# Kernel tuning notes

Measured on AMD Instinct MI355X. Metric: run time of the kernel, lower is better.

The kernel has to match this reference:

```python
import jax, jax.numpy as jnp
import numpy as np

INF = 1e30  # sentinel for 'unreached' cost
MAX_ITERS = 512


def setup_inputs() -> dict:
    key = jax.random.key(0)
    img = jax.random.uniform(key, (3, 2048, 2048), dtype=jnp.float32)
    return {"img": img}


def _sobel_mag(gray):
    # gray: [H,W] -> gradient magnitude [H,W] (the 'processing_filter')
    kx = jnp.array([[-1.0, 0.0, 1.0], [-2.0, 0.0, 2.0], [-1.0, 0.0, 1.0]], gray.dtype)
    k = jnp.stack([kx, kx.T])[:, None]  # [2,1,3,3]
    g = jax.lax.conv_general_dilated(gray[None, None], k, (1, 1), 'SAME')[0]  # [2,H,W]
    return jnp.sqrt(g[0] ** 2 + g[1] ** 2)


def _neighbor_min(c):
    # min over 4-connected neighbors, INF padding at borders
    big_r = jnp.full((1, c.shape[1]), INF, c.dtype)
    big_c = jnp.full((c.shape[0], 1), INF, c.dtype)
    n = jnp.concatenate([big_r, c[:-1]], 0)
    s = jnp.concatenate([c[1:], big_r], 0)
    w = jnp.concatenate([big_c, c[:, :-1]], 1)
    e = jnp.concatenate([c[:, 1:], big_c], 1)
    return jnp.minimum(jnp.minimum(n, s), jnp.minimum(w, e))


def _relax(cost, img):
    # minimax-path (flood-level) relaxation: cost[p] = min(cost[p], max(min_nbr_cost, img[p]))
    return jnp.minimum(cost, jnp.maximum(_neighbor_min(cost), img))


def _watershed2(img, markers):
    # marker-based watershed on topography `img` with labels {1,2}.
    # Label of p = argmin over seed sets of the minimax path cost (flooding level),
    # which matches skimage.segmentation.watershed region assignment (4-connectivity).
    c1 = jnp.where(markers == 1, img, jnp.float32(INF))
    c2 = jnp.where(markers == 2, img, jnp.float32(INF))

    def cond(st):
        _, _, i, ch = st
        return jnp.logical_and(ch, i < MAX_ITERS)

    def body(st):
        c1, c2, i, _ = st
        n1 = _relax(c1, img)
        n2 = _relax(c2, img)
        ch = jnp.logical_or(jnp.any(n1 < c1), jnp.any(n2 < c2))
        return n1, n2, i + 1, ch

    c1, c2, _, _ = jax.lax.while_loop(cond, body, (c1, c2, jnp.int32(0), jnp.bool_(True)))
    return jnp.where(c2 < c1, jnp.float32(2.0), jnp.float32(1.0))


def _forward(img):
    gray = jnp.einsum('chw,c->hw', img, jnp.array([0.2989, 0.587, 0.114], img.dtype))
    filter_res = _sobel_mag(gray)  # [H,W]
    q_hi = jnp.quantile(filter_res, 0.9925)
    q_lo = jnp.quantile(filter_res, 0.9825)
    # torch sets 2 first, then 1, so pixels satisfying both end up as 1
    markers = jnp.where(filter_res <= q_lo, 1, jnp.where(filter_res >= q_hi, 2, 0))
    labels = _watershed2(gray, markers)[None]  # [1,H,W], values in {1,2}
    labels = labels - labels.min()
    return labels / labels.max()


def reference(img):
    return _forward(img)
```

## Files before the change

kernel.cpp:

```cpp
#include <hip/hip_runtime.h>
#include <hip/hip_cooperative_groups.h>

#define HH 2048
#define WW 2048
#define NPX (HH*WW)
#define INFV 1e30f
#define TS 128
#define NT 16
#define NTL 256
#define CY 32

namespace cg = cooperative_groups;

__device__ __forceinline__ void BARL(){
  __builtin_amdgcn_sched_barrier(0);
  asm volatile("s_waitcnt lgkmcnt(0)" ::: "memory");
  __builtin_amdgcn_s_barrier();
  __builtin_amdgcn_sched_barrier(0);
}

__device__ __forceinline__ float sobel_at(const float* __restrict__ g, int y, int x){
  float a00,a01,a02,a10,a12,a20,a21,a22;
  if (y>0 && y<HH-1 && x>0 && x<WW-1){
    const float* p = g + (size_t)(y-1)*WW + x;
    a00=p[-1]; a01=p[0]; a02=p[1];
    p += WW;   a10=p[-1];          a12=p[1];
    p += WW;   a20=p[-1]; a21=p[0]; a22=p[1];
  } else {
    auto at=[&](int yy,int xx)->float{
      return (yy<0||yy>=HH||xx<0||xx>=WW)?0.0f:g[(size_t)yy*WW+xx];
    };
    a00=at(y-1,x-1); a01=at(y-1,x); a02=at(y-1,x+1);
    a10=at(y,  x-1);                a12=at(y,  x+1);
    a20=at(y+1,x-1); a21=at(y+1,x); a22=at(y+1,x+1);
  }
  float gx = __fadd_rn(__fadd_rn(__fsub_rn(a02,a00), __fmul_rn(2.0f,__fsub_rn(a12,a10))), __fsub_rn(a22,a20));
  float gy = __fadd_rn(__fadd_rn(__fsub_rn(a20,a00), __fmul_rn(2.0f,__fsub_rn(a21,a01))), __fsub_rn(a22,a02));
  return sqrtf(__fadd_rn(__fmul_rn(gx,gx),__fmul_rn(gy,gy)));
}

__global__ void gray_kernel(const float* __restrict__ img, float* __restrict__ gray){
  const float* R=img; const float* G=img+NPX; const float* B=img+2*(size_t)NPX;
  for (int i=blockIdx.x*blockDim.x+threadIdx.x; i<NPX; i+=gridDim.x*blockDim.x){
    gray[i] = __fadd_rn(__fadd_rn(__fmul_rn(0.2989f,R[i]),__fmul_rn(0.587f,G[i])),__fmul_rn(0.114f,B[i]));
  }
}

__global__ void sobel_hist1(const float* __restrict__ gray, float* __restrict__ fr,
                            unsigned* __restrict__ hist){
  __shared__ unsigned h[4*2048];
  for (int i=threadIdx.x;i<4*2048;i+=blockDim.x) h[i]=0;
  __syncthreads();
  const int rep=(threadIdx.x&3)*2048;
  for (int i=blockIdx.x*blockDim.x+threadIdx.x; i<NPX; i+=gridDim.x*blockDim.x){
    int y=i>>11, x=i&(WW-1);
    float f=sobel_at(gray,y,x);
    fr[i]=f;
    unsigned key=__float_as_uint(f);
    atomicAdd(&h[rep+(key>>21)],1u);
  }
  __syncthreads();
  for (int i=threadIdx.x;i<2048;i+=blockDim.x){
    unsigned s=h[i]+h[i+2048]+h[i+4096]+h[i+6144];
    if (s) atomicAdd(&hist[i],s);
  }
}

__global__ void hist_l2(const float* __restrict__ fr, const unsigned* __restrict__ sel1,
                        unsigned* __restrict__ hist2){
  __shared__ unsigned h[4*2048];
  __shared__ unsigned sb[4];
  if (threadIdx.x<4) sb[threadIdx.x]=sel1[threadIdx.x];
  for (int i=threadIdx.x;i<4*2048;i+=blockDim.x) h[i]=0;
  __syncthreads();
  for (int i=blockIdx.x*blockDim.x+threadIdx.x; i<NPX; i+=gridDim.x*blockDim.x){
    unsigned key=__float_as_uint(fr[i]);
    unsigned b=key>>21, sub=(key>>10)&0x7FFu;
    #pragma unroll
    for (int k=0;k<4;++k) if (b==sb[k]) atomicAdd(&h[k*2048+sub],1u);
  }
  __syncthreads();
  for (int i=threadIdx.x;i<4*2048;i+=blockDim.x){ unsigned s=h[i]; if (s) atomicAdd(&hist2[i],s); }
}

__global__ void hist_l3(const float* __restrict__ fr, const unsigned* __restrict__ sel1,
                        const unsigned* __restrict__ sel2, unsigned* __restrict__ hist3){
  __shared__ unsigned h[4*1024];
  __shared__ unsigned pf[4];
  if (threadIdx.x<4) pf[threadIdx.x]=(sel1[threadIdx.x]<<11)|sel2[threadIdx.x];
  for (int i=threadIdx.x;i<4*1024;i+=blockDim.x) h[i]=0;
  __syncthreads();
  for (int i=blockIdx.x*blockDim.x+threadIdx.x; i<NPX; i+=gridDim.x*blockDim.x){
    unsigned key=__float_as_uint(fr[i]);
    unsigned p22=key>>10, sub=key&0x3FFu;
    #pragma unroll
    for (int k=0;k<4;++k) if (p22==pf[k]) atomicAdd(&h[k*1024+sub],1u);
  }
  __syncthreads();
  for (int i=threadIdx.x;i<4*1024;i+=blockDim.x){ unsigned s=h[i]; if (s) atomicAdd(&hist3[i],s); }
}

__global__ void scan_l1(const unsigned* __restrict__ hist, unsigned* __restrict__ sel1,
                        unsigned* __restrict__ rem1){
  __shared__ unsigned part[1024];
  const int t=threadIdx.x;
  unsigned a=hist[2*t], b=hist[2*t+1];
  part[t]=a+b; __syncthreads();
  for (int off=1;off<1024;off<<=1){
    unsigned add=(t>=off)?part[t-off]:0u; __syncthreads();
    part[t]+=add; __syncthreads();
  }
  unsigned before=(t>0)?part[t-1]:0u;
  const unsigned R[4]={4120902u,4120903u,4162845u,4162846u};
  unsigned cum=before;
  #pragma unroll
  for (int i=0;i<4;++i) if (R[i]>=cum && R[i]<cum+a){ sel1[i]=2*t;   rem1[i]=R[i]-cum; }
  cum+=a;
  #pragma unroll
  for (int i=0;i<4;++i) if (R[i]>=cum && R[i]<cum+b){ sel1[i]=2*t+1; rem1[i]=R[i]-cum; }
}

__global__ void scan_l2(const unsigned* __restrict__ hist2, const unsigned* __restrict__ rem1,
                        unsigned* __restrict__ sel2, unsigned* __restrict__ rem2){
  __shared__ unsigned part[1024];
  const int t=threadIdx.x;
  for (int i=0;i<4;++i){
    const unsigned* hh=hist2+i*2048;
    unsigned a=hh[2*t], b=hh[2*t+1];
    part[t]=a+b; __syncthreads();
    for (int off=1;off<1024;off<<=1){
      unsigned add=(t>=off)?part[t-off]:0u; __syncthreads();
      part[t]+=add; __syncthreads();
    }
    unsigned before=(t>0)?part[t-1]:0u;
    unsigned r=rem1[i], cum=before;
    if (r>=cum && r<cum+a){ sel2[i]=2*t;   rem2[i]=r-cum; }
    cum+=a;
    if (r>=cum && r<cum+b){ sel2[i]=2*t+1; rem2[i]=r-cum; }
    __syncthreads();
  }
}

__global__ void scan_l3(const unsigned* __restrict__ hist3, const unsigned* __restrict__ sel1,
                        const unsigned* __restrict__ sel2, const unsigned* __restrict__ rem2,
                        float* __restrict__ scal){
  __shared__ unsigned part[1024];
  __shared__ float vals[4];
  const int t=threadIdx.x;
  for (int i=0;i<4;++i){
    unsigned c=hist3[i*1024+t];
    part[t]=c; __syncthreads();
    for (int off=1;off<1024;off<<=1){
      unsigned add=(t>=off)?part[t-off]:0u; __syncthreads();
      part[t]+=add; __syncthreads();
    }
    unsigned before=(t>0)?part[t-1]:0u;
    unsigned r=rem2[i];
    if (r>=before && r<before+c){
      unsigned key=(sel1[i]<<21)|(sel2[i]<<10)|(unsigned)t;
      vals[i]=__uint_as_float(key);
    }
    __syncthreads();
  }
  if (t==0){
    scal[0]=__fadd_rn(__fmul_rn(vals[0],0.25f),__fmul_rn(vals[1],0.75f));
    scal[1]=__fadd_rn(__fmul_rn(vals[2],0.25f),__fmul_rn(vals[3],0.75f));
  }
}

__global__ void init_cost(const float* __restrict__ gray, const float* frbuf,
                          const float* __restrict__ scal,
                          float* c1out, float* __restrict__ c2out){
  const float qlo=scal[0], qhi=scal[1];
  for (int i=blockIdx.x*blockDim.x+threadIdx.x; i<NPX; i+=gridDim.x*blockDim.x){
    float f=frbuf[i];
    float g=gray[i];
    bool m1 = (f<=qlo);
    bool m2 = (!m1) && (f>=qhi);
    c1out[i] = m1 ? g : INFV;
    c2out[i] = (m1|m2) ? g : INFV;
  }
}


#define HSCAN_LR(va,vb,gA,gB,hl) do{ \
  float ql_=gA[j], qh_=va[j]; \
  qh_=fminf(vb[j],fmaxf(gB[j],qh_)); ql_=fmaxf(gB[j],ql_); \
  _Pragma("unroll") \
  for (int d_=1;d_<64;d_<<=1){ \
    float pl_=__shfl_up(ql_,(unsigned)d_), ph_=__shfl_up(qh_,(unsigned)d_); \
    if (c>=d_){ qh_=fminf(qh_,fmaxf(ql_,ph_)); ql_=fmaxf(ql_,pl_); } \
  } \
  float E_=fminf(qh_,fmaxf(ql_,(hl))); \
  float In_=__shfl_up(E_,1u); if(c==0) In_=(hl); \
  float na_=fminf(va[j],fmaxf(gA[j],In_)); if(na_<va[j]){va[j]=na_;ch=true;} \
  float nb_=fminf(vb[j],fmaxf(gB[j],na_)); if(nb_<vb[j]){vb[j]=nb_;ch=true;} \
}while(0)

#define HSCAN_RL(va,vb,gA,gB,hr) do{ \
  float ql_=gB[j], qh_=vb[j]; \
  qh_=fminf(va[j],fmaxf(gA[j],qh_)); ql_=fmaxf(gA[j],ql_); \
  _Pragma("unroll") \
  for (int d_=1;d_<64;d_<<=1){ \
    float pl_=__shfl_down(ql_,(unsigned)d_), ph_=__shfl_down(qh_,(unsigned)d_); \
    if (c+d_<64){ qh_=fminf(qh_,fmaxf(ql_,ph_)); ql_=fmaxf(ql_,pl_); } \
  } \
  float E_=fminf(qh_,fmaxf(ql_,(hr))); \
  float In_=__shfl_down(E_,1u); if(c==63) In_=(hr); \
  float nb_=fminf(vb[j],fmaxf(gB[j],In_)); if(nb_<vb[j]){vb[j]=nb_;ch=true;} \
  float na_=fminf(va[j],fmaxf(gA[j],nb_)); if(na_<va[j]){va[j]=na_;ch=true;} \
}while(0)

#define VCOMP_DN(va,gA,Larr,Harr,XX) { float ql_=gA[0], qh_=va[0]; \
  _Pragma("unroll") for (int jj_=1;jj_<8;++jj_){ qh_=fminf(va[jj_],fmaxf(gA[jj_],qh_)); ql_=fmaxf(gA[jj_],ql_);} \
  Larr[w][XX]=ql_; Harr[w][XX]=qh_; }

#define VCOMP_UP(va,gA,Larr,Harr,XX) { float ql_=gA[7], qh_=va[7]; \
  _Pragma("unroll") for (int jj_=6;jj_>=0;--jj_){ qh_=fminf(va[jj_],fmaxf(gA[jj_],qh_)); ql_=fmaxf(gA[jj_],ql_);} \
  Larr[w][XX]=ql_; Harr[w][XX]=qh_; }

#define VAPPLY_DN(va,gA,Larr,XX) { float In_=Larr[w][XX]; \
  _Pragma("unroll") for (int jj_=0;jj_<8;++jj_){ float nv_=fminf(va[jj_],fmaxf(In_,gA[jj_])); if(nv_<va[jj_]){va[jj_]=nv_;ch=true;} In_=nv_; } }

#define VAPPLY_UP(va,gA,Larr,XX) { float In_=Larr[w][XX]; \
  _Pragma("unroll") for (int jj_=7;jj_>=0;--jj_){ float nv_=fminf(va[jj_],fmaxf(In_,gA[jj_])); if(nv_<va[jj_]){va[jj_]=nv_;ch=true;} In_=nv_; } }

#define CHAIN_DN(Harr,Larr,HT) { float E=HALO[HT][x]; \
  _Pragma("unroll") for (int b_=0;b_<16;++b_){ float I=E; E=fminf(Harr[b_][x],fmaxf(Larr[b_][x],I)); Larr[b_][x]=I; } }

#define CHAIN_UP(Harr,Larr,HB) { float E=HALO[HB][x]; \
  _Pragma("unroll") for (int b_=15;b_>=0;--b_){ float I=E; E=fminf(Harr[b_][x],fmaxf(Larr[b_][x],I)); Larr[b_][x]=I; } }

#define HFIELD(va,vb,IHL,IHR) do{ \
  _Pragma("unroll") \
  for (int j=0;j<8;++j){ \
    const int r_=(w<<3)|j; \
    const float hl=HALO[IHL][r_], hr=HALO[IHR][r_]; \
    { float la_=__shfl_up(vb[j],1u); if(c==0) la_=hl; \
      bool p_=__any((fminf(va[j],fmaxf(la_,ga[j]))<va[j])||(fminf(vb[j],fmaxf(va[j],gb[j]))<vb[j])); \
      if (p_){ HSCAN_LR(va,vb,ga,gb,hl); } } \
    { float ra_=__shfl_down(va[j],1u); if(c==63) ra_=hr; \
      bool p_=__any((fminf(vb[j],fmaxf(ra_,gb[j]))<vb[j])||(fminf(va[j],fmaxf(vb[j],ga[j]))<va[j])); \
      if (p_){ HSCAN_RL(va,vb,ga,gb,hr); } } \
  } \
}while(0)

#define ASTORE(p,v) __hip_atomic_store((p),(v),__ATOMIC_RELAXED,__HIP_MEMORY_SCOPE_AGENT)
#define ALOAD(p)    __hip_atomic_load((p),__ATOMIC_RELAXED,__HIP_MEMORY_SCOPE_AGENT)

__global__ void __launch_bounds__(1024,4)
tile_solve(float* __restrict__ c1g, float* __restrict__ cg, const float* __restrict__ grayg)
{
  __shared__ float DNL1[16][128], DNH1[16][128], DNL2[16][128], DNH2[16][128];
  __shared__ float UPL1[16][128], UPH1[16][128], UPL2[16][128], UPH2[16][128];
  __shared__ float HALO[8][128];
  __shared__ int VN1[2],HN1[2],VN2[2],HN2[2];
  const int tid=threadIdx.x, w=tid>>6, c=tid&63;
  const int oty=blockIdx.x>>5, otx=blockIdx.x&31;
  const int wy0=oty*64-32, wx0=otx*64-32, x0=c<<1;
  HALO[tid>>7][tid&127]=INFV;
  if (tid==0){ VN1[0]=1;HN1[0]=1;VN2[0]=1;HN2[0]=1;
               VN1[1]=0;HN1[1]=0;VN2[1]=0;HN2[1]=0; }
  float v1a[8],v1b[8],v2a[8],v2b[8],ga[8],gb[8];
  const int gx=wx0+x0;
  const bool cok=(gx>=0)&&(gx+1<WW);
  #pragma unroll
  for (int j=0;j<8;++j){
    const int gy=wy0+(w<<3)+j;
    const bool rok=(gy>=0)&&(gy<HH);
    if (rok&&cok){
      const size_t b=(size_t)gy*WW+gx;
      float2 t1=*(const float2*)(c1g+b);
      float2 t2=*(const float2*)(cg+b);
      float2 tg=*(const float2*)(grayg+b);
      v1a[j]=t1.x; v1b[j]=t1.y; v2a[j]=t2.x; v2b[j]=t2.y; ga[j]=tg.x; gb[j]=tg.y;
    } else if (rok){
      const bool aok=(gx>=0)&&(gx<WW), bok=(gx+1>=0)&&(gx+1<WW);
      const size_t b=(size_t)gy*WW;
      v1a[j]=aok?c1g[b+gx]:INFV;   v1b[j]=bok?c1g[b+gx+1]:INFV;
      v2a[j]=aok?cg [b+gx]:INFV;   v2b[j]=bok?cg [b+gx+1]:INFV;
      ga [j]=aok?grayg[b+gx]:INFV; gb [j]=bok?grayg[b+gx+1]:INFV;
    } else {
      v1a[j]=INFV;v1b[j]=INFV;v2a[j]=INFV;v2b[j]=INFV;ga[j]=INFV;gb[j]=INFV;
    }
  }
  __syncthreads();
  for (int cyc=0; cyc<64; ++cyc){
    const int cur=cyc&1, nxt=cur^1;
    const int vn1=VN1[cur], hn1=HN1[cur], vn2=VN2[cur], hn2=HN2[cur];
    if (!(vn1|hn1|vn2|hn2)) break;
    if (vn1){
      VCOMP_DN(v1a,ga,DNL1,DNH1,x0) VCOMP_DN(v1b,gb,DNL1,DNH1,x0+1)
      VCOMP_UP(v1a,ga,UPL1,UPH1,x0) VCOMP_UP(v1b,gb,UPL1,UPH1,x0+1)
    }
    if (vn2){
      VCOMP_DN(v2a,ga,DNL2,DNH2,x0) VCOMP_DN(v2b,gb,DNL2,DNH2,x0+1)
      VCOMP_UP(v2a,ga,UPL2,UPH2,x0) VCOMP_UP(v2b,gb,UPL2,UPH2,x0+1)
    }
    __syncthreads();
    if (w<8){
      const int x=((w&1)<<6)|c;
      const bool go=(w>>2)?(vn2!=0):(vn1!=0);
      if (go){
        switch(w>>1){
          case 0: CHAIN_DN(DNH1,DNL1,0) break;
          case 1: CHAIN_UP(UPH1,UPL1,2) break;
          case 2: CHAIN_DN(DNH2,DNL2,1) break;
          default:CHAIN_UP(UPH2,UPL2,3) break;
        }
      }
    }
    __syncthreads();
    if (vn1){ bool ch=false;
      VAPPLY_DN(v1a,ga,DNL1,x0) VAPPLY_DN(v1b,gb,DNL1,x0+1)
      VAPPLY_UP(v1a,ga,UPL1,x0) VAPPLY_UP(v1b,gb,UPL1,x0+1)
      if (ch) HN1[nxt]=1;
    }
    if (hn1){ bool ch=false;
      HFIELD(v1a,v1b,4,6);
      if (ch) VN1[nxt]=1;
    }
    if (vn2){ bool ch=false;
      VAPPLY_DN(v2a,ga,DNL2,x0) VAPPLY_DN(v2b,gb,DNL2,x0+1)
      VAPPLY_UP(v2a,ga,UPL2,x0) VAPPLY_UP(v2b,gb,UPL2,x0+1)
      if (ch) HN2[nxt]=1;
    }
    if (hn2){ bool ch=false;
      HFIELD(v2a,v2b,5,7);
      if (ch) VN2[nxt]=1;
    }
    if (tid==0){ VN1[cur]=0; HN1[cur]=0; VN2[cur]=0; HN2[cur]=0; }
    __syncthreads();
  }
  if (w>=4 && w<12 && c>=16 && c<48){
    #pragma unroll
    for (int j=0;j<8;++j){
      const int gy=wy0+(w<<3)+j;
      const size_t b=(size_t)gy*WW+gx;
      float2 o1; o1.x=v1a[j]; o1.y=v1b[j];
      float2 o2; o2.x=v2a[j]; o2.y=v2b[j];
      *(float2*)(c1g+b)=o1;
      *(float2*)(cg +b)=o2;
    }
  }
}

#define CYCLE(HV,CUR,NXT) do{ \
  if (hsrc){ \
    if (HV < HALO[harr][hx]){ \
      HALO[harr][hx]=HV; \
      if (harr<4){ if (harr&1) VN2[NXT]=1; else VN1[NXT]=1; } \
      else       { if (harr&1) HN2[NXT]=1; else HN1[NXT]=1; } \
    } \
    HV=ALOAD(hsrc); \
  } \
  const int vn1=VN1[CUR], hn1=HN1[CUR], vn2=VN2[CUR], hn2=HN2[CUR]; \
  if (!(vn1|hn1|vn2|hn2)){ \
    BARL(); \
  } else { \
    if (vn1){ \
      VCOMP_DN(v1a,ga,DNL1,DNH1,x0) VCOMP_DN(v1b,gb,DNL1,DNH1,x0+1) \
      VCOMP_UP(v1a,ga,UPL1,UPH1,x0) VCOMP_UP(v1b,gb,UPL1,UPH1,x0+1) \
    } \
    if (vn2){ \
      VCOMP_DN(v2a,ga,DNL2,DNH2,x0) VCOMP_DN(v2b,gb,DNL2,DNH2,x0+1) \
      VCOMP_UP(v2a,ga,UPL2,UPH2,x0) VCOMP_UP(v2b,gb,UPL2,UPH2,x0+1) \
    } \
    BARL(); \
    if (w<8){ \
      const int x=((w&1)<<6)|c; \
      const bool go = (w>>2) ? (vn2!=0) : (vn1!=0); \
      if (go){ \
        switch(w>>1){ \
          case 0: CHAIN_DN(DNH1,DNL1,0) break; \
          case 1: CHAIN_UP(UPH1,UPL1,2) break; \
          case 2: CHAIN_DN(DNH2,DNL2,1) break; \
          default:CHAIN_UP(UPH2,UPL2,3) break; \
        } \
      } \
    } \
    BARL(); \
    bool chf1=false, chf2=false; \
    if (vn1){ bool ch=false; \
      VAPPLY_DN(v1a,ga,DNL1,x0) VAPPLY_DN(v1b,gb,DNL1,x0+1) \
      VAPPLY_UP(v1a,ga,UPL1,x0) VAPPLY_UP(v1b,gb,UPL1,x0+1) \
      if (ch){ chf1=true; HN1[NXT]=1; } \
    } \
    if (hn1){ bool ch=false; \
      HFIELD(v1a,v1b,4,6); \
      if (ch){ chf1=true; VN1[NXT]=1; } \
    } \
    if (vn2){ bool ch=false; \
      VAPPLY_DN(v2a,ga,DNL2,x0) VAPPLY_DN(v2b,gb,DNL2,x0+1) \
      VAPPLY_UP(v2a,ga,UPL2,x0) VAPPLY_UP(v2b,gb,UPL2,x0+1) \
      if (ch){ chf2=true; HN2[NXT]=1; } \
    } \
    if (hn2){ bool ch=false; \
      HFIELD(v2a,v2b,5,7); \
      if (ch){ chf2=true; VN2[NXT]=1; } \
    } \
    if (chf1|chf2){ \
      if (w==0){ const int eb=(tile*4+0)*128; \
        if(chf1){ ASTORE(EB1+eb+x0,v1a[0]); ASTORE(EB1+eb+x0+1,v1b[0]); } \
        if(chf2){ ASTORE(EB2+eb+x0,v2a[0]); ASTORE(EB2+eb+x0+1,v2b[0]); } } \
      if (w==15){ const int eb=(tile*4+1)*128; \
        if(chf1){ ASTORE(EB1+eb+x0,v1a[7]); ASTORE(EB1+eb+x0+1,v1b[7]); } \
        if(chf2){ ASTORE(EB2+eb+x0,v2a[7]); ASTORE(EB2+eb+x0+1,v2b[7]); } } \
      if (c==0){ const int eb=(tile*4+2)*128+(w<<3); \
        _Pragma("unroll") \
        for (int j=0;j<8;++j){ if(chf1)ASTORE(EB1+eb+j,v1a[j]); if(chf2)ASTORE(EB2+eb+j,v2a[j]); } } \
      if (c==63){ const int eb=(tile*4+3)*128+(w<<3); \
        _Pragma("unroll") \
        for (int j=0;j<8;++j){ if(chf1)ASTORE(EB1+eb+j,v1b[j]); if(chf2)ASTORE(EB2+eb+j,v2b[j]); } } \
      wflag=1; \
    } \
    if (tid==0){ VN1[CUR]=0; HN1[CUR]=0; VN2[CUR]=0; HN2[CUR]=0; } \
    BARL(); \
  } \
}while(0)

__global__ void __launch_bounds__(1024,4)
ws_solve(float* __restrict__ c1g, const float* __restrict__ grayg, float* outg,
         int* __restrict__ flagIt)
{
  __shared__ float DNL1[16][128], DNH1[16][128], DNL2[16][128], DNH2[16][128];
  __shared__ float UPL1[16][128], UPH1[16][128], UPL2[16][128], UPH2[16][128];
  __shared__ float HALO[8][128];
  __shared__ int VN1[2],HN1[2],VN2[2],HN2[2];
  __shared__ int wflag;
  cg::grid_group grid = cg::this_grid();
  const int tid=threadIdx.x, w=tid>>6, c=tid&63;
  const int xcd=blockIdx.x&7, idx=blockIdx.x>>3;
  const int tx=((xcd&3)<<2)|(idx&3), ty=((xcd>>2)<<3)|(idx>>2);
  const int tile=ty*NT+tx;
  const int by=ty*TS, bx=tx*TS, x0=c<<1;
  float* EB1=outg;
  float* EB2=outg+(NTL*4*128);

  const int hx=tid&127, harr=tid>>7;
  const float* hsrc=nullptr;
  {
    const float* EB=(harr&1)?EB2:EB1;
    switch(harr>>1){
      case 0: if (ty>0)    hsrc=EB+((tile-NT)*4+1)*128+hx; break;
      case 1: if (ty<NT-1) hsrc=EB+((tile+NT)*4+0)*128+hx; break;
      case 2: if (tx>0)    hsrc=EB+((tile-1)*4+3)*128+hx;  break;
      default:if (tx<NT-1) hsrc=EB+((tile+1)*4+2)*128+hx;  break;
    }
  }

  float v1a[8],v1b[8],v2a[8],v2b[8],ga[8],gb[8];
  {
    size_t base=(size_t)(by+(w<<3))*WW + bx + x0;
    #pragma unroll
    for (int j=0;j<8;++j){
      float2 t1=*(const float2*)(c1g+base);
      float2 t2=*(const float2*)(outg+base);
      float2 tg=*(const float2*)(grayg+base);
      v1a[j]=t1.x; v1b[j]=t1.y; v2a[j]=t2.x; v2b[j]=t2.y; ga[j]=tg.x; gb[j]=tg.y;
      base+=(size_t)WW;
    }
  }
  grid.sync();

  if (w==0){ const int eb=(tile*4+0)*128;
    ASTORE(EB1+eb+x0,v1a[0]); ASTORE(EB1+eb+x0+1,v1b[0]);
    ASTORE(EB2+eb+x0,v2a[0]); ASTORE(EB2+eb+x0+1,v2b[0]); }
  if (w==15){ const int eb=(tile*4+1)*128;
    ASTORE(EB1+eb+x0,v1a[7]); ASTORE(EB1+eb+x0+1,v1b[7]);
    ASTORE(EB2+eb+x0,v2a[7]); ASTORE(EB2+eb+x0+1,v2b[7]); }
  if (c==0){ const int eb=(tile*4+2)*128+(w<<3);
    #pragma unroll
    for (int j=0;j<8;++j){ ASTORE(EB1+eb+j,v1a[j]); ASTORE(EB2+eb+j,v2a[j]); } }
  if (c==63){ const int eb=(tile*4+3)*128+(w<<3);
    #pragma unroll
    for (int j=0;j<8;++j){ ASTORE(EB1+eb+j,v1b[j]); ASTORE(EB2+eb+j,v2b[j]); } }
  HALO[harr][hx]=INFV;
  if (tid==0){ VN1[0]=1;HN1[0]=1;VN2[0]=1;HN2[0]=1;
               VN1[1]=0;HN1[1]=0;VN2[1]=0;HN2[1]=0; wflag=0; }
  __threadfence();
  grid.sync();

  float hvA=INFV, hvB=INFV;
  if (hsrc){ hvA=ALOAD(hsrc); hvB=ALOAD(hsrc); }

  for (int win=0; win<96; ++win){
    for (int cyc=0; cyc<CY; cyc+=2){
      CYCLE(hvA,0,1);
      CYCLE(hvB,1,0);
    }
    if (tid==0 && wflag) atomicMax(flagIt,win+1);
    __threadfence();
    grid.sync();
    int fv=ALOAD(flagIt);
    if (fv<=win) break;
    if (tid==0) wflag=0;
    __syncthreads();
  }
  {
    size_t base=(size_t)(by+(w<<3))*WW + bx + x0;
    #pragma unroll
    for (int j=0;j<8;++j){
      float2 o; o.x=(v2a[j]<v1a[j])?1.0f:0.0f; o.y=(v2b[j]<v1b[j])?1.0f:0.0f;
      *(float2*)(outg+base)=o;
      base+=(size_t)WW;
    }
  }
}

extern "C" void kernel_launch(void* const* d_in, const int* in_sizes, int n_in,
                              void* d_out, int out_size, void* d_ws, size_t ws_size,
                              hipStream_t stream)
{
  const float* img=(const float*)d_in[0];
  float* out=(float*)d_out;
  char* wsb=(char*)d_ws;
  float* gray=(float*)wsb;
  float* c1  =(float*)(wsb + (size_t)NPX*4);
  unsigned* meta=(unsigned*)(wsb + (size_t)NPX*8);
  float* c2 = out;

  unsigned* hist1=meta;
  unsigned* hist2=meta+2048;
  unsigned* hist3=meta+10240;
  unsigned* sel1 =meta+14336;
  unsigned* rem1 =meta+14340;
  unsigned* sel2 =meta+14344;
  unsigned* rem2 =meta+14348;
  float*    scal =(float*)(meta+14352);
  int*      flagIt=(int*)(meta+14354);

  hipMemsetAsync(meta, 0, 14355*sizeof(unsigned), stream);
  hipLaunchKernelGGL(gray_kernel, dim3(4096), dim3(256), 0, stream, img, gray);
  hipLaunchKernelGGL(sobel_hist1, dim3(1024), dim3(256), 0, stream, gray, c1, hist1);
  hipLaunchKernelGGL(scan_l1, dim3(1), dim3(1024), 0, stream, hist1, sel1, rem1);
  hipLaunchKernelGGL(hist_l2, dim3(1024), dim3(256), 0, stream, c1, sel1, hist2);
  hipLaunchKernelGGL(scan_l2, dim3(1), dim3(1024), 0, stream, hist2, rem1, sel2, rem2);
  hipLaunchKernelGGL(hist_l3, dim3(1024), dim3(256), 0, stream, c1, sel1, sel2, hist3);
  hipLaunchKernelGGL(scan_l3, dim3(1), dim3(1024), 0, stream, hist3, sel1, sel2, rem2, scal);
  hipLaunchKernelGGL(init_cost, dim3(4096), dim3(256), 0, stream, gray, c1, scal, c1, c2);

  hipLaunchKernelGGL(tile_solve, dim3(1024), dim3(1024), 0, stream, c1, c2, gray);

  void* args[]={ (void*)&c1,(void*)&gray,(void*)&out,(void*)&flagIt };
  (void)hipLaunchCooperativeKernel(ws_solve, dim3(NTL), dim3(1024), args, 0, stream);
}
```

Measured before the change: 562.1 us.

## Track per-wave dirty bitmasks to skip unchanged vertical segment compute and apply

Replaces the per-tile vertical-needed flags with per-wave dirty bitmasks (VD) and a per-segment change mask from the chain pass (ECH). Only waves whose column segments changed recompute their segment summaries, and only waves whose incoming chain values changed re-apply the vertical scan. The chain outputs go to new shared arrays (EDN/EUP) so they can be compared with the previous values. This aims to cut redundant vertical work in sparse late iterations. In exchange it adds 32KB more LDS per block, extra __any votes and shared atomics, which could hurt occupancy under the 4-block launch bound.

```diff
diff --git a/kernel.cpp b/kernel.cpp
--- a/kernel.cpp
+++ b/kernel.cpp
@@ -230,6 +230,22 @@
 
 #define CHAIN_UP(Harr,Larr,HB) { float E=HALO[HB][x]; \
   _Pragma("unroll") for (int b_=15;b_>=0;--b_){ float I=E; E=fminf(Harr[b_][x],fmaxf(Larr[b_][x],I)); Larr[b_][x]=I; } }
+
+#define CHAINC_DN(Harr,Larr,Earr,HT,ECHV) { \
+  float E=HALO[HT][x]; unsigned m_=0; \
+  _Pragma("unroll") for (int b_=0;b_<16;++b_){ \
+    float I_=E; E=fminf(Harr[b_][x],fmaxf(Larr[b_][x],I_)); \
+    if (__any(I_!=Earr[b_][x])) m_|=(1u<<b_); \
+    Earr[b_][x]=I_; } \
+  if (c==0 && m_) atomicOr(&ECHV,(int)m_); }
+
+#define CHAINC_UP(Harr,Larr,Earr,HB,ECHV) { \
+  float E=HALO[HB][x]; unsigned m_=0; \
+  _Pragma("unroll") for (int b_=15;b_>=0;--b_){ \
+    float I_=E; E=fminf(Harr[b_][x],fmaxf(Larr[b_][x],I_)); \
+    if (__any(I_!=Earr[b_][x])) m_|=(1u<<b_); \
+    Earr[b_][x]=I_; } \
+  if (c==0 && m_) atomicOr(&ECHV,(int)m_); }
 
 #define HFIELD(va,vb,IHL,IHR) do{ \
   _Pragma("unroll") \
@@ -355,64 +371,76 @@
     HV=ALOAD(hsrc); \
   } \
   const int vn1=VN1[CUR], hn1=HN1[CUR], vn2=VN2[CUR], hn2=HN2[CUR]; \
-  if (!(vn1|hn1|vn2|hn2)){ \
+  const unsigned vd1=(unsigned)VD1s, vd2=(unsigned)VD2s; \
+  if (!(vn1|hn1|vn2|hn2|(int)(vd1|vd2))){ \
     BARL(); \
   } else { \
-    if (vn1){ \
+     \
+    if ((vd1>>w)&1){ \
       VCOMP_DN(v1a,ga,DNL1,DNH1,x0) VCOMP_DN(v1b,gb,DNL1,DNH1,x0+1) \
       VCOMP_UP(v1a,ga,UPL1,UPH1,x0) VCOMP_UP(v1b,gb,UPL1,UPH1,x0+1) \
     } \
-    if (vn2){ \
+    if ((vd2>>w)&1){ \
       VCOMP_DN(v2a,ga,DNL2,DNH2,x0) VCOMP_DN(v2b,gb,DNL2,DNH2,x0+1) \
       VCOMP_UP(v2a,ga,UPL2,UPH2,x0) VCOMP_UP(v2b,gb,UPL2,UPH2,x0+1) \
     } \
+    if (tid==0){ ECH1s=0; ECH2s=0; } \
     BARL(); \
+     \
     if (w<8){ \
       const int x=((w&1)<<6)|c; \
-      const bool go = (w>>2) ? (vn2!=0) : (vn1!=0); \
-      if (go){ \
-        switch(w>>1){ \
-          case 0: CHAIN_DN(DNH1,DNL1,0) break; \
-          case 1: CHAIN_UP(UPH1,UPL1,2) break; \
-          case 2: CHAIN_DN(DNH2,DNL2,1) break; \
-          default:CHAIN_UP(UPH2,UPL2,3) break; \
-        } \
+      switch(w>>1){ \
+        case 0: if (vn1|(int)vd1) CHAINC_DN(DNH1,DNL1,EDN1,0,ECH1s) break; \
+        case 1: if (vn1|(int)vd1) CHAINC_UP(UPH1,UPL1,EUP1,2,ECH1s) break; \
+        case 2: if (vn2|(int)vd2) CHAINC_DN(DNH2,DNL2,EDN2,1,ECH2s) break; \
+        default:if (vn2|(int)vd2) CHAINC_UP(UPH2,UPL2,EUP2,3,ECH2s) break; \
       } \
     } \
+    if (tid==0){ VD1s=0; VD2s=0; } \
     BARL(); \
-    bool chf1=false, chf2=false; \
-    if (vn1){ bool ch=false; \
-      VAPPLY_DN(v1a,ga,DNL1,x0) VAPPLY_DN(v1b,gb,DNL1,x0+1) \
-      VAPPLY_UP(v1a,ga,UPL1,x0) VAPPLY_UP(v1b,gb,UPL1,x0+1) \
-      if (ch){ chf1=true; HN1[NXT]=1; } \
-    } \
-    if (hn1){ bool ch=false; \
-      HFIELD(v1a,v1b,4,6); \
-      if (ch){ chf1=true; VN1[NXT]=1; } \
-    } \
-    if (vn2){ bool ch=false; \
-      VAPPLY_DN(v2a,ga,DNL2,x0) VAPPLY_DN(v2b,gb,DNL2,x0+1) \
-      VAPPLY_UP(v2a,ga,UPL2,x0) VAPPLY_UP(v2b,gb,UPL2,x0+1) \
-      if (ch){ chf2=true; HN2[NXT]=1; } \
-    } \
-    if (hn2){ bool ch=false; \
-      HFIELD(v2a,v2b,5,7); \
-      if (ch){ chf2=true; VN2[NXT]=1; } \
-    } \
-    if (chf1|chf2){ \
+     \
+    const unsigned am1=((unsigned)ECH1s)|vd1, am2=((unsigned)ECH2s)|vd2; \
+    bool pf1=false, pf2=false; \
+    { bool ch=false; \
+      if ((am1>>w)&1){ \
+        VAPPLY_DN(v1a,ga,EDN1,x0) VAPPLY_DN(v1b,gb,EDN1,x0+1) \
+        VAPPLY_UP(v1a,ga,EUP1,x0) VAPPLY_UP(v1b,gb,EUP1,x0+1) \
+      } \
+      bool vch=__any(ch); \
+      ch=false; \
+      if (hn1){ HFIELD(v1a,v1b,4,6); } \
+      bool hch=__any(ch); \
+      if ((vch|hch) && c==0) atomicOr(&VD1s,1<<w); \
+      if (vch) HN1[NXT]=1; \
+      pf1 = vch|hch; \
+    } \
+    { bool ch=false; \
+      if ((am2>>w)&1){ \
+        VAPPLY_DN(v2a,ga,EDN2,x0) VAPPLY_DN(v2b,gb,EDN2,x0+1) \
+        VAPPLY_UP(v2a,ga,EUP2,x0) VAPPLY_UP(v2b,gb,EUP2,x0+1) \
+      } \
+      bool vch=__any(ch); \
+      ch=false; \
+      if (hn2){ HFIELD(v2a,v2b,5,7); } \
+      bool hch=__any(ch); \
+      if ((vch|hch) && c==0) atomicOr(&VD2s,1<<w); \
+      if (vch) HN2[NXT]=1; \
+      pf2 = vch|hch; \
+    } \
+    if (pf1|pf2){ \
       if (w==0){ const int eb=(tile*4+0)*128; \
-        if(chf1){ ASTORE(EB1+eb+x0,v1a[0]); ASTORE(EB1+eb+x0+1,v1b[0]); } \
-        if(chf2){ ASTORE(EB2+eb+x0,v2a[0]); ASTORE(EB2+eb+x0+1,v2b[0]); } } \
+        if(pf1){ ASTORE(EB1+eb+x0,v1a[0]); ASTORE(EB1+eb+x0+1,v1b[0]); } \
+        if(pf2){ ASTORE(EB2+eb+x0,v2a[0]); ASTORE(EB2+eb+x0+1,v2b[0]); } } \
       if (w==15){ const int eb=(tile*4+1)*128; \
-        if(chf1){ ASTORE(EB1+eb+x0,v1a[7]); ASTORE(EB1+eb+x0+1,v1b[7]); } \
-        if(chf2){ ASTORE(EB2+eb+x0,v2a[7]); ASTORE(EB2+eb+x0+1,v2b[7]); } } \
+        if(pf1){ ASTORE(EB1+eb+x0,v1a[7]); ASTORE(EB1+eb+x0+1,v1b[7]); } \
+        if(pf2){ ASTORE(EB2+eb+x0,v2a[7]); ASTORE(EB2+eb+x0+1,v2b[7]); } } \
       if (c==0){ const int eb=(tile*4+2)*128+(w<<3); \
         _Pragma("unroll") \
-        for (int j=0;j<8;++j){ if(chf1)ASTORE(EB1+eb+j,v1a[j]); if(chf2)ASTORE(EB2+eb+j,v2a[j]); } } \
+        for (int j=0;j<8;++j){ if(pf1)ASTORE(EB1+eb+j,v1a[j]); if(pf2)ASTORE(EB2+eb+j,v2a[j]); } } \
       if (c==63){ const int eb=(tile*4+3)*128+(w<<3); \
         _Pragma("unroll") \
-        for (int j=0;j<8;++j){ if(chf1)ASTORE(EB1+eb+j,v1b[j]); if(chf2)ASTORE(EB2+eb+j,v2b[j]); } } \
-      wflag=1; \
+        for (int j=0;j<8;++j){ if(pf1)ASTORE(EB1+eb+j,v1b[j]); if(pf2)ASTORE(EB2+eb+j,v2b[j]); } } \
+      if (c==1) wflag=1; \
     } \
     if (tid==0){ VN1[CUR]=0; HN1[CUR]=0; VN2[CUR]=0; HN2[CUR]=0; } \
     BARL(); \
@@ -425,8 +453,10 @@
 {
   __shared__ float DNL1[16][128], DNH1[16][128], DNL2[16][128], DNH2[16][128];
   __shared__ float UPL1[16][128], UPH1[16][128], UPL2[16][128], UPH2[16][128];
+  __shared__ float EDN1[16][128], EUP1[16][128], EDN2[16][128], EUP2[16][128];
   __shared__ float HALO[8][128];
   __shared__ int VN1[2],HN1[2],VN2[2],HN2[2];
+  __shared__ int VD1s, VD2s, ECH1s, ECH2s;
   __shared__ int wflag;
   cg::grid_group grid = cg::this_grid();
   const int tid=threadIdx.x, w=tid>>6, c=tid&63;
@@ -477,7 +507,8 @@
     for (int j=0;j<8;++j){ ASTORE(EB1+eb+j,v1b[j]); ASTORE(EB2+eb+j,v2b[j]); } }
   HALO[harr][hx]=INFV;
   if (tid==0){ VN1[0]=1;HN1[0]=1;VN2[0]=1;HN2[0]=1;
-               VN1[1]=0;HN1[1]=0;VN2[1]=0;HN2[1]=0; wflag=0; }
+               VN1[1]=0;HN1[1]=0;VN2[1]=0;HN2[1]=0;
+               VD1s=0xFFFF; VD2s=0xFFFF; ECH1s=0; ECH2s=0; wflag=0; }
   __threadfence();
   grid.sync();
 
@@ -489,7 +520,7 @@
       CYCLE(hvA,0,1);
       CYCLE(hvB,1,0);
     }
-    if (tid==0 && wflag) atomicMax(flagIt,win+1);
+    if (tid==0 && (wflag || (VD1s|VD2s))) atomicMax(flagIt,win+1);
     __threadfence();
     grid.sync();
     int fv=ALOAD(flagIt);
```

Result: slower. 578.4 us (+2.9%).
